# Performance work log

Measured on AMD Instinct MI355X. Metric: run time of the kernel, lower is better.

## Reference

```python
import jax, jax.numpy as jnp
import numpy as np


def setup_inputs() -> dict:
    key = jax.random.key(0)
    k1, k2, k3 = jax.random.split(key, 3)
    B, DIM, H, Wd = 32, 512, 64, 64
    K, DQ = 64, 3
    features = jax.random.normal(k1, (B, DIM, H, Wd), dtype=jnp.float32)
    query = jax.random.normal(k2, (B, DQ, H, Wd), dtype=jnp.float32)
    # Ensemble of K 1x1 convs (no bias): weight [K, dim_query, dim], scaled like conv init
    W = jax.random.normal(k3, (K, DQ, DIM), dtype=jnp.float32) * (1.0 / np.sqrt(DIM))
    return {"features": features, "query": query, "W": W}


def reference(features, query, W):
    B = query.shape[0]
    # ensemble 1x1 conv: key_values [k, b, q, h, w]
    kv = jnp.einsum('kqd,bdhw->kbqhw', W, features)
    # rearrange 'k b ... -> b k ...'
    kv_b = jnp.transpose(kv, (1, 0, 2, 3, 4))          # [b, k, q, h, w]
    q_flat = query.reshape(B, 1, -1)                    # [b, 1, N]
    kv_flat = kv_b.reshape(B, kv_b.shape[1], -1)        # [b, k, N]
    # torch.cdist (p=2) between [b,1,N] and [b,k,N] -> [b,k]
    diff = q_flat - kv_flat
    distance = jnp.sqrt(jnp.sum(diff * diff, axis=-1))  # [b, k]
    codes = jnp.argmin(distance, axis=-1)               # [b]
    # batched gather of selected key_values
    idx = codes[:, None, None, None, None]
    sel_key_values = jnp.take_along_axis(kv_b, idx, axis=1)[:, 0]  # [b, q, h, w]
    commit_loss = jnp.mean((sel_key_values - query) ** 2)
    return sel_key_values, codes, commit_loss
```

## Files before the change

### kernel.cpp

```cpp
#include <hip/hip_runtime.h>
#include <hip/hip_bf16.h>
#include <hip/hip_fp16.h>

#define BN   32
#define DIMK 512
#define HW   4096
#define KK   64
#define DQ   3
#define RR   192
#define NT   128
#define NBLK (HW / NT)

typedef _Float16 half8  __attribute__((ext_vector_type(8)));
typedef float    f32x2  __attribute__((ext_vector_type(2)));
typedef float    f32x4  __attribute__((ext_vector_type(4)));
typedef short    short8 __attribute__((ext_vector_type(8)));

#define A16_OFF    0
#define A16_BYTES  (RR * DIMK * 2)
#define PART_OFF   196608
#define PART_BYTES (BN * NBLK * KK * 4)
#define KV_OFF     524288
#define KV_BYTES   ((size_t)BN * RR * HW * 2)

#define OUT_SEL    ((size_t)BN * DQ * HW)
#define OUT_LOSS   (OUT_SEL + BN)

__global__ void init_kernel(const float* __restrict__ Wsrc,
                            _Float16* __restrict__ A16,
                            float* __restrict__ out) {
  int gid = blockIdx.x * 256 + threadIdx.x;
  if (gid < RR * DIMK) A16[gid] = (_Float16)Wsrc[gid];
  if (gid == 0)        out[OUT_LOSS] = 0.f;
}

template <bool STORE>
__global__ __launch_bounds__(256) void gemm_dist_kernel(
    const float* __restrict__ f, const float* __restrict__ query,
    const _Float16* __restrict__ A16, __hip_bfloat16* __restrict__ kv,
    float* __restrict__ partial) {
  __shared__ __align__(16) _Float16 Blds[2][4][NT][8];
  __shared__ float qlds[DQ][NT];
  __shared__ float rowsum[RR];

  const int t  = threadIdx.x;
  const int w  = t >> 6;
  const int l  = t & 63;
  const int lq = l >> 4;
  const int ln = l & 15;
  const int b  = blockIdx.y;
  const int n0 = blockIdx.x * NT;

  for (int s = t; s < DQ * NT; s += 256) {
    int q = s / NT, n = s % NT;
    qlds[q][n] = query[((size_t)b * DQ + q) * HW + n0 + n];
  }

  f32x4 acc[3][8];
#pragma unroll
  for (int mt = 0; mt < 3; mt++)
#pragma unroll
    for (int nt = 0; nt < 8; nt++) acc[mt][nt] = (f32x4)0.f;

  const int bn  = t & 63;
  const int bkb = t >> 6;

  f32x2 bpre[8];
  half8 apre[3];

  const int arow = w * 48 + ln;

  auto loadB = [&](int kk) {
    const float* fp = f + ((size_t)b * DIMK + kk * 32 + bkb * 8) * HW + n0 + 2 * bn;
#pragma unroll
    for (int j = 0; j < 8; j++) bpre[j] = *(const f32x2*)&fp[(size_t)j * HW];
  };
  auto loadA = [&](int kk) {
#pragma unroll
    for (int mt = 0; mt < 3; mt++)
      apre[mt] = *(const half8*)&A16[(arow + mt * 16) * DIMK + kk * 32 + lq * 8];
  };
  auto stageB = [&](int buf) {
    half8 h0, h1;
#pragma unroll
    for (int j = 0; j < 8; j++) {
      h0[j] = (_Float16)bpre[j][0];
      h1[j] = (_Float16)bpre[j][1];
    }
    *(half8*)&Blds[buf][bkb][2 * bn][0]     = h0;
    *(half8*)&Blds[buf][bkb][2 * bn + 1][0] = h1;
  };

  loadA(0);
  loadB(0);
  stageB(0);
  for (int kk = 0; kk < DIMK / 32; kk++) {
    const int cur = kk & 1;
    __syncthreads();
    if (kk < DIMK / 32 - 1) loadB(kk + 1);

    half8 af[3];
#pragma unroll
    for (int mt = 0; mt < 3; mt++) af[mt] = apre[mt];
    if (kk < DIMK / 32 - 1) loadA(kk + 1);

#pragma unroll
    for (int h = 0; h < 2; h++) {
      half8 bf[4];
#pragma unroll
      for (int n4 = 0; n4 < 4; n4++)
        bf[n4] = *(const half8*)&Blds[cur][lq][h * 64 + n4 * 16 + ln][0];
#pragma unroll
      for (int mt = 0; mt < 3; mt++)
#pragma unroll
        for (int n4 = 0; n4 < 4; n4++)
          acc[mt][h * 4 + n4] = __builtin_amdgcn_mfma_f32_16x16x32_f16(
              af[mt], bf[n4], acc[mt][h * 4 + n4], 0, 0, 0);
    }
    if (kk < DIMK / 32 - 1) stageB(cur ^ 1);
  }

  float rs[3][4];
#pragma unroll
  for (int mt = 0; mt < 3; mt++)
#pragma unroll
    for (int i = 0; i < 4; i++) rs[mt][i] = 0.f;

#pragma unroll
  for (int mt = 0; mt < 3; mt++) {
#pragma unroll
    for (int i = 0; i < 4; i++) {
      int r = w * 48 + mt * 16 + lq * 4 + i;
      int q = r % 3;
#pragma unroll
      for (int nt = 0; nt < 8; nt++) {
        int n = nt * 16 + ln;
        float c = acc[mt][nt][i];
        if (STORE) kv[((size_t)b * RR + r) * HW + n0 + n] = __float2bfloat16(c);
        float d = c - qlds[q][n];
        rs[mt][i] += d * d;
      }
    }
  }
#pragma unroll
  for (int mt = 0; mt < 3; mt++)
#pragma unroll
    for (int i = 0; i < 4; i++) {
      float v = rs[mt][i];
      v += __shfl_xor(v, 1, 64);
      v += __shfl_xor(v, 2, 64);
      v += __shfl_xor(v, 4, 64);
      v += __shfl_xor(v, 8, 64);
      rs[mt][i] = v;
    }
  if (ln < 12) {
    int mt = ln >> 2, i = ln & 3;
    rowsum[w * 48 + mt * 16 + lq * 4 + i] = rs[mt][i];
  }
  __syncthreads();
  if (t < KK)
    partial[((size_t)b * NBLK + blockIdx.x) * KK + t] =
        rowsum[3 * t] + rowsum[3 * t + 1] + rowsum[3 * t + 2];
}

__global__ __launch_bounds__(256) void gather_kernel(
    const __hip_bfloat16* __restrict__ kv, const float* __restrict__ query,
    const float* __restrict__ partial, float* __restrict__ out) {
  int b = blockIdx.x, t = threadIdx.x;
  __shared__ float dsum[KK];
  __shared__ int scode;
  __shared__ float red[4];
  if (t < KK) {
    float s = 0.f;
    for (int x = 0; x < NBLK; x++) s += partial[((size_t)b * NBLK + x) * KK + t];
    dsum[t] = s;
  }
  __syncthreads();
  if (t == 0) {
    float best = dsum[0]; int bi = 0;
    for (int k = 1; k < KK; k++)
      if (dsum[k] < best) { best = dsum[k]; bi = k; }
    scode = bi;
    out[OUT_SEL + b] = (float)bi;
  }
  __syncthreads();
  int code = scode;
  const short8* src = (const short8*)(kv + ((size_t)b * RR + code * DQ) * HW);
  const f32x4*  qp  = (const f32x4*)(query + (size_t)b * DQ * HW);
  f32x4*        op  = (f32x4*)(out + (size_t)b * DQ * HW);
  float lsum = 0.f;
  for (int c = t; c < DQ * HW / 8; c += 256) {
    short8 v = src[c];
    f32x4 o0, o1;
#pragma unroll
    for (int j = 0; j < 4; j++) {
      unsigned u0 = ((unsigned)(unsigned short)v[j]) << 16;
      unsigned u1 = ((unsigned)(unsigned short)v[4 + j]) << 16;
      o0[j] = __builtin_bit_cast(float, u0);
      o1[j] = __builtin_bit_cast(float, u1);
    }
    f32x4 q0 = qp[2 * c], q1 = qp[2 * c + 1];
    op[2 * c] = o0; op[2 * c + 1] = o1;
#pragma unroll
    for (int j = 0; j < 4; j++) {
      float d0 = o0[j] - q0[j], d1 = o1[j] - q1[j];
      lsum += d0 * d0 + d1 * d1;
    }
  }
  for (int off = 1; off < 64; off <<= 1) lsum += __shfl_xor(lsum, off, 64);
  if ((t & 63) == 0) red[t >> 6] = lsum;
  __syncthreads();
  if (t == 0)
    atomicAdd(&out[OUT_LOSS],
              (red[0] + red[1] + red[2] + red[3]) * (1.f / (float)(BN * DQ * HW)));
}

__global__ __launch_bounds__(256) void recompute_kernel(
    const float* __restrict__ f, const float* __restrict__ query,
    const float* __restrict__ Wsrc, const float* __restrict__ partial,
    float* __restrict__ out) {
  int b = blockIdx.y, t = threadIdx.x;
  int hw = blockIdx.x * 256 + t;
  __shared__ float dsum[KK];
  __shared__ int scode;
  __shared__ float red[4];
  if (t < KK) {
    float s = 0.f;
    for (int x = 0; x < NBLK; x++) s += partial[((size_t)b * NBLK + x) * KK + t];
    dsum[t] = s;
  }
  __syncthreads();
  if (t == 0) {
    float best = dsum[0]; int bi = 0;
    for (int k = 1; k < KK; k++)
      if (dsum[k] < best) { best = dsum[k]; bi = k; }
    scode = bi;
    if (blockIdx.x == 0) out[OUT_SEL + b] = (float)bi;
  }
  __syncthreads();
  int code = scode;
  const float* w0 = Wsrc + (size_t)code * DQ * DIMK;
  const float* fp = f + (size_t)b * DIMK * HW + hw;
  float a0 = 0.f, a1 = 0.f, a2 = 0.f;
  for (int d = 0; d < DIMK; d++) {
    float fv = fp[(size_t)d * HW];
    a0 += w0[d] * fv;
    a1 += w0[DIMK + d] * fv;
    a2 += w0[2 * DIMK + d] * fv;
  }
  const float* qp = query + (size_t)b * DQ * HW;
  float* op = out + (size_t)b * DQ * HW;
  op[hw] = a0; op[HW + hw] = a1; op[2 * HW + hw] = a2;
  float d0 = a0 - qp[hw], d1 = a1 - qp[HW + hw], d2 = a2 - qp[2 * HW + hw];
  float lsum = d0 * d0 + d1 * d1 + d2 * d2;
  for (int off = 1; off < 64; off <<= 1) lsum += __shfl_xor(lsum, off, 64);
  if ((t & 63) == 0) red[t >> 6] = lsum;
  __syncthreads();
  if (t == 0)
    atomicAdd(&out[OUT_LOSS],
              (red[0] + red[1] + red[2] + red[3]) * (1.f / (float)(BN * DQ * HW)));
}

extern "C" void kernel_launch(void* const* d_in, const int* in_sizes, int n_in,
                              void* d_out, int out_size, void* d_ws, size_t ws_size,
                              hipStream_t stream) {
  const float* f     = (const float*)d_in[0];
  const float* query = (const float*)d_in[1];
  const float* Wsrc  = (const float*)d_in[2];
  float* out = (float*)d_out;
  char*  ws  = (char*)d_ws;

  _Float16*        A16     = (_Float16*)(ws + A16_OFF);
  float*           partial = (float*)(ws + PART_OFF);
  __hip_bfloat16*  kv      = (__hip_bfloat16*)(ws + KV_OFF);

  const bool store = ws_size >= (size_t)KV_OFF + KV_BYTES;

  init_kernel<<<384, 256, 0, stream>>>(Wsrc, A16, out);
  if (store) {
    gemm_dist_kernel<true><<<dim3(NBLK, BN), 256, 0, stream>>>(f, query, A16, kv, partial);
    gather_kernel<<<BN, 256, 0, stream>>>(kv, query, partial, out);
  } else {
    gemm_dist_kernel<false><<<dim3(NBLK, BN), 256, 0, stream>>>(f, query, A16, nullptr, partial);
    recompute_kernel<<<dim3(HW / 256, BN), 256, 0, stream>>>(f, query, Wsrc, partial, out);
  }
}
```

Before: 390.2 us.

## Prefetch feature tiles two iterations ahead and stage weights through LDS

The feature (B operand) global loads now use two register sets, so loads for iteration k+2 are issued while iteration k computes, which deepens the prefetch and hides more HBM latency. The weight tiles are loaded cooperatively with coalesced 16-byte reads, written to a double-buffered LDS array, and read back per wave, instead of each wave fetching its fragments straight from global memory. The cost is more registers for the second feature set, extra LDS traffic and capacity, and possibly lower occupancy.

```diff
diff --git a/kernel.cpp b/kernel.cpp
--- a/kernel.cpp
+++ b/kernel.cpp
@@ -10,6 +10,7 @@
 #define RR   192
 #define NT   128
 #define NBLK (HW / NT)
+#define KITER (DIMK / 32)
 
 typedef _Float16 half8  __attribute__((ext_vector_type(8)));
 typedef float    f32x2  __attribute__((ext_vector_type(2)));
@@ -39,6 +40,7 @@
     const float* __restrict__ f, const float* __restrict__ query,
     const _Float16* __restrict__ A16, __hip_bfloat16* __restrict__ kv,
     float* __restrict__ partial) {
+  __shared__ __align__(16) _Float16 Alds[2][RR][40];
   __shared__ __align__(16) _Float16 Blds[2][4][NT][8];
   __shared__ float qlds[DQ][NT];
   __shared__ float rowsum[RR];
@@ -65,44 +67,57 @@
   const int bn  = t & 63;
   const int bkb = t >> 6;
 
-  f32x2 bpre[8];
+  f32x2 set0[8], set1[8];
   half8 apre[3];
 
-  const int arow = w * 48 + ln;
-
-  auto loadB = [&](int kk) {
+  auto loadB = [&](int kk, f32x2 (&dst)[8]) {
     const float* fp = f + ((size_t)b * DIMK + kk * 32 + bkb * 8) * HW + n0 + 2 * bn;
 #pragma unroll
-    for (int j = 0; j < 8; j++) bpre[j] = *(const f32x2*)&fp[(size_t)j * HW];
+    for (int j = 0; j < 8; j++) dst[j] = *(const f32x2*)&fp[(size_t)j * HW];
   };
   auto loadA = [&](int kk) {
 #pragma unroll
-    for (int mt = 0; mt < 3; mt++)
-      apre[mt] = *(const half8*)&A16[(arow + mt * 16) * DIMK + kk * 32 + lq * 8];
-  };
-  auto stageB = [&](int buf) {
+    for (int i = 0; i < 3; i++) {
+      int s = t + i * 256;
+      int m = s >> 2, oct = s & 3;
+      apre[i] = *(const half8*)&A16[m * DIMK + kk * 32 + oct * 8];
+    }
+  };
+  auto stageA = [&](int buf) {
+#pragma unroll
+    for (int i = 0; i < 3; i++) {
+      int s = t + i * 256;
+      int m = s >> 2, oct = s & 3;
+      *(half8*)&Alds[buf][m][oct * 8] = apre[i];
+    }
+  };
+  auto stageB = [&](const f32x2 (&src)[8], int buf) {
     half8 h0, h1;
 #pragma unroll
     for (int j = 0; j < 8; j++) {
-      h0[j] = (_Float16)bpre[j][0];
-      h1[j] = (_Float16)bpre[j][1];
+      h0[j] = (_Float16)src[j][0];
+      h1[j] = (_Float16)src[j][1];
     }
     *(half8*)&Blds[buf][bkb][2 * bn][0]     = h0;
     *(half8*)&Blds[buf][bkb][2 * bn + 1][0] = h1;
   };
 
+  loadB(0, set0);
   loadA(0);
-  loadB(0);
-  stageB(0);
-  for (int kk = 0; kk < DIMK / 32; kk++) {
+  loadB(1, set1);
+  stageA(0);
+  stageB(set0, 0);
+
+  auto iter = [&](int kk, f32x2 (&SA)[8], const f32x2 (&SB)[8]) {
     const int cur = kk & 1;
     __syncthreads();
-    if (kk < DIMK / 32 - 1) loadB(kk + 1);
+    if (kk < KITER - 1) loadA(kk + 1);
+    if (kk < KITER - 2) loadB(kk + 2, SA);
 
     half8 af[3];
 #pragma unroll
-    for (int mt = 0; mt < 3; mt++) af[mt] = apre[mt];
-    if (kk < DIMK / 32 - 1) loadA(kk + 1);
+    for (int mt = 0; mt < 3; mt++)
+      af[mt] = *(const half8*)&Alds[cur][w * 48 + mt * 16 + ln][lq * 8];
 
 #pragma unroll
     for (int h = 0; h < 2; h++) {
@@ -117,7 +132,15 @@
           acc[mt][h * 4 + n4] = __builtin_amdgcn_mfma_f32_16x16x32_f16(
               af[mt], bf[n4], acc[mt][h * 4 + n4], 0, 0, 0);
     }
-    if (kk < DIMK / 32 - 1) stageB(cur ^ 1);
+    if (kk < KITER - 1) {
+      stageA(cur ^ 1);
+      stageB(SB, cur ^ 1);
+    }
+  };
+
+  for (int kk2 = 0; kk2 < KITER / 2; kk2++) {
+    iter(2 * kk2,     set0, set1);
+    iter(2 * kk2 + 1, set1, set0);
   }
 
   float rs[3][4];
```

Measured after the change: 382.2 us. 1.02x faster.
